# Kernel optimization log

Hardware: AMD Instinct MI355X
Metric: run time of the kernel (lower is better)

Reference implementation:

```python
import jax, jax.numpy as jnp
import numpy as np

MEL_BINS = 128
NUM_KEYS = 88
FMAX = 8000.0
HPS_HARMONICS = 3
THRESH_PCT = 85.0


def _mel_frequencies(n_mels: int, fmax: float, fmin: float = 0.0) -> np.ndarray:
    """Replicates librosa.mel_frequencies (Slaney scale, htk=False)."""
    f_sp = 200.0 / 3.0
    min_log_hz = 1000.0
    min_log_mel = min_log_hz / f_sp
    logstep = np.log(6.4) / 27.0

    def hz_to_mel(f):
        f = np.asarray(f, dtype=np.float64)
        lin = f / f_sp
        log = min_log_mel + np.log(np.maximum(f, 1e-10) / min_log_hz) / logstep
        return np.where(f >= min_log_hz, log, lin)

    def mel_to_hz(m):
        m = np.asarray(m, dtype=np.float64)
        lin = f_sp * m
        log = min_log_hz * np.exp(logstep * (m - min_log_mel))
        return np.where(m >= min_log_mel, log, lin)

    mels = np.linspace(hz_to_mel(fmin), hz_to_mel(fmax), n_mels)
    return mel_to_hz(mels)


def _compute_key_bins() -> np.ndarray:
    mel_freqs = _mel_frequencies(MEL_BINS, FMAX)  # (128,)
    pitches = np.arange(NUM_KEYS) + 21            # MIDI 21..108
    freqs = 440.0 * 2.0 ** ((pitches - 69) / 12.0)
    bins = np.argmin(np.abs(mel_freqs[None, :] - freqs[:, None]), axis=1)
    return np.minimum(bins, MEL_BINS - 1).astype(np.int32)


def setup_inputs() -> dict:
    key = jax.random.key(0)
    B, M, T = 16, MEL_BINS, 16384
    mel = jax.random.normal(key, (B, M, T), dtype=jnp.float32)
    key_bins = jnp.asarray(_compute_key_bins(), dtype=jnp.int32)  # (88,)
    return {"mel": mel, "key_bins": key_bins}


def reference(mel, key_bins):
    # mel: (B, M, T); key_bins: (88,) int32
    spec = jnp.exp(mel)                       # (B, M, T)
    hps = spec
    for h in range(2, HPS_HARMONICS + 1):
        ds = spec[:, ::h, :]                  # (B, ceil(M/h), T)
        L = ds.shape[1]
        hps = hps.at[:, :L, :].multiply(ds)   # harmonic product into low bins
    energies = jnp.take(hps, key_bins, axis=1)            # (B, 88, T)
    thresh = jnp.percentile(energies, THRESH_PCT, axis=1,
                            keepdims=True)                 # (B, 1, T)
    probs = (energies >= thresh).astype(jnp.float32)       # (B, 88, T)
    return (probs, probs)
```

## Files before the change

### kernel.cpp

```cpp
#include <hip/hip_runtime.h>

#define LOG2_T 14
#define NKEYS  88
#define NB     16
#define DMAX   64
#define TOPK   14

__global__ __launch_bounds__(256) void tsp_kernel(
    const float* __restrict__ mel,
    const int*   __restrict__ key_bins,
    float*       __restrict__ out)
{
    __shared__ int s_bin[DMAX];
    __shared__ int s_mult[DMAX];
    __shared__ int s_start[DMAX];
    __shared__ int s_Dsh;

    if (threadIdx.x == 0) {
        int D = 0, prev = -1;
        for (int k = 0; k < NKEYS; ++k) {
            int bin = key_bins[k];
            if (bin != prev && D < DMAX) {
                s_bin[D] = bin; s_mult[D] = 0; s_start[D] = k; prev = bin; ++D;
            }
            s_mult[D - 1] += 1;
        }
        for (int d = D; d < DMAX; ++d) { s_bin[d] = 0; s_mult[d] = 0; s_start[d] = NKEYS; }
        s_Dsh = D;
    }
    __syncthreads();

    const int tid = threadIdx.x;
    const int bid = blockIdx.x;
    const int b   = bid >> 6;
    const int t   = ((bid & 63) << 8) + tid;
    const int D   = s_Dsh;

    const float* melb = mel + ((size_t)b << 21);

    float e[DMAX];
    #pragma unroll
    for (int d = 0; d < DMAX; ++d) {
        const int bin = __builtin_amdgcn_readfirstlane(s_bin[d]);
        const int b1  = (2 * bin < 128) ? 2 * bin : 127;
        const int b2  = (3 * bin < 128) ? 3 * bin : 127;
        const float x0 = melb[((size_t)bin << LOG2_T) + t];
        const float x1 = melb[((size_t)b1  << LOG2_T) + t];
        const float x2 = melb[((size_t)b2  << LOG2_T) + t];
        float v = expf(x0);
        v *= (bin < 64) ? expf(x1) : 1.0f;
        v *= (bin < 43) ? expf(x2) : 1.0f;
        e[d] = (d < D) ? v : 0.0f;
    }

    float tv[TOPK];
    float cur = 1e38f;
    #pragma unroll
    for (int i = 0; i < TOPK; ++i) {
        float m = -1.0f;
        #pragma unroll
        for (int d = 0; d < DMAX; ++d) {
            const float c = (e[d] < cur) ? e[d] : -1.0f;
            m = fmaxf(m, c);
        }
        tv[i] = m;
        cur = m;
    }

    int W[TOPK];
    #pragma unroll
    for (int i = 0; i < TOPK; ++i) W[i] = 0;
    #pragma unroll
    for (int d = 0; d < DMAX; ++d) {
        const int mlt = s_mult[d];
        const float ed = e[d];
        #pragma unroll
        for (int i = 0; i < TOPK; ++i)
            W[i] += (ed >= tv[i]) ? mlt : 0;
    }
    float thr = tv[TOPK - 1];
    #pragma unroll
    for (int i = TOPK - 2; i >= 0; --i)
        thr = (W[i] >= TOPK) ? tv[i] : thr;

    float*       out2    = out + ((size_t)(NB * NKEYS) << LOG2_T);
    const size_t colbase = (((size_t)b * NKEYS) << LOG2_T) + t;
    #pragma unroll
    for (int d = 0; d < DMAX; ++d) {
        const int ks = __builtin_amdgcn_readfirstlane(s_start[d]);
        const int ke = __builtin_amdgcn_readfirstlane(s_start[d] + s_mult[d]);
        const float p = (e[d] >= thr) ? 1.0f : 0.0f;
        for (int k = ks; k < ke; ++k) {
            const size_t idx = colbase + ((size_t)k << LOG2_T);
            out[idx]  = p;
            out2[idx] = p;
        }
    }
}

extern "C" void kernel_launch(void* const* d_in, const int* in_sizes, int n_in,
                              void* d_out, int out_size, void* d_ws, size_t ws_size,
                              hipStream_t stream) {
    const float* mel = (const float*)d_in[0];
    const int*   kb  = (const int*)d_in[1];
    float*       out = (float*)d_out;
    tsp_kernel<<<dim3(1024), dim3(256), 0, stream>>>(mel, kb, out);
}
```

Measured before the change: 302.1 us.

## Batch global loads in chunks, parallelize bin setup, tree-reduce top-k max

Measured after the change: 359.5 us. 1.19x slower.

```diff
diff --git a/kernel.cpp b/kernel.cpp
--- a/kernel.cpp
+++ b/kernel.cpp
@@ -5,8 +5,9 @@
 #define NB     16
 #define DMAX   64
 #define TOPK   14
+#define CHUNK  16
 
-__global__ __launch_bounds__(256) void tsp_kernel(
+__global__ __launch_bounds__(256, 4) void tsp_kernel(
     const float* __restrict__ mel,
     const int*   __restrict__ key_bins,
     float*       __restrict__ out)
@@ -14,57 +15,96 @@
     __shared__ int s_bin[DMAX];
     __shared__ int s_mult[DMAX];
     __shared__ int s_start[DMAX];
-    __shared__ int s_Dsh;
+    __shared__ int s_wcnt[4];
 
-    if (threadIdx.x == 0) {
-        int D = 0, prev = -1;
-        for (int k = 0; k < NKEYS; ++k) {
-            int bin = key_bins[k];
-            if (bin != prev && D < DMAX) {
-                s_bin[D] = bin; s_mult[D] = 0; s_start[D] = k; prev = bin; ++D;
-            }
-            s_mult[D - 1] += 1;
+    const int tid  = threadIdx.x;
+    const int lane = tid & 63;
+    const int wid  = tid >> 6;
+
+    bool nf = false; int mybin = 0;
+    if (tid < NKEYS) {
+        mybin = key_bins[tid];
+        const int prev = tid ? key_bins[tid - 1] : -1;
+        nf = (mybin != prev);
+    }
+    const unsigned long long bm = __ballot(nf);
+    const int pre = __popcll(bm & ((1ull << lane) - 1ull));
+    if (lane == 0) s_wcnt[wid] = __popcll(bm);
+    __syncthreads();
+    if (nf) {
+        int r = pre;
+        for (int w = 0; w < wid; ++w) r += s_wcnt[w];
+        s_start[r] = tid;
+        s_bin[r]   = mybin;
+    }
+    const int D = s_wcnt[0] + s_wcnt[1];
+    __syncthreads();
+    if (tid < DMAX) {
+        if (tid < D) {
+            const int nxt = (tid == D - 1) ? NKEYS : s_start[tid + 1];
+            s_mult[tid] = nxt - s_start[tid];
+        } else {
+            s_bin[tid] = 0; s_mult[tid] = 0; s_start[tid] = NKEYS;
         }
-        for (int d = D; d < DMAX; ++d) { s_bin[d] = 0; s_mult[d] = 0; s_start[d] = NKEYS; }
-        s_Dsh = D;
     }
     __syncthreads();
 
-    const int tid = threadIdx.x;
-    const int bid = blockIdx.x;
-    const int b   = bid >> 6;
-    const int t   = ((bid & 63) << 8) + tid;
-    const int D   = s_Dsh;
-
+    const int bidx = blockIdx.x;
+    const int b    = bidx >> 6;
+    const int t    = ((bidx & 63) << 8) + tid;
     const float* melb = mel + ((size_t)b << 21);
 
     float e[DMAX];
     #pragma unroll
-    for (int d = 0; d < DMAX; ++d) {
-        const int bin = __builtin_amdgcn_readfirstlane(s_bin[d]);
-        const int b1  = (2 * bin < 128) ? 2 * bin : 127;
-        const int b2  = (3 * bin < 128) ? 3 * bin : 127;
-        const float x0 = melb[((size_t)bin << LOG2_T) + t];
-        const float x1 = melb[((size_t)b1  << LOG2_T) + t];
-        const float x2 = melb[((size_t)b2  << LOG2_T) + t];
-        float v = expf(x0);
-        v *= (bin < 64) ? expf(x1) : 1.0f;
-        v *= (bin < 43) ? expf(x2) : 1.0f;
-        e[d] = (d < D) ? v : 0.0f;
+    for (int c = 0; c < DMAX; c += CHUNK) {
+        float x0[CHUNK], x1[CHUNK], x2[CHUNK];
+        int   bns[CHUNK];
+        #pragma unroll
+        for (int i = 0; i < CHUNK; ++i) {
+            const int d  = c + i;
+            const int bn = __builtin_amdgcn_readfirstlane(s_bin[d]);
+            const int b1 = (2 * bn < 128) ? 2 * bn : 127;
+            const int b2 = (3 * bn < 128) ? 3 * bn : 127;
+            bns[i] = bn;
+            x0[i] = melb[((size_t)bn << LOG2_T) + t];
+            x1[i] = melb[((size_t)b1 << LOG2_T) + t];
+            x2[i] = melb[((size_t)b2 << LOG2_T) + t];
+        }
+        #pragma unroll
+        for (int i = 0; i < CHUNK; ++i) {
+            const int d  = c + i;
+            const int bn = bns[i];
+            float v = expf(x0[i]);
+            v *= (bn < 64) ? expf(x1[i]) : 1.0f;
+            v *= (bn < 43) ? expf(x2[i]) : 1.0f;
+            e[d] = (d < D) ? v : 0.0f;
+        }
     }
 
     float tv[TOPK];
-    float cur = 1e38f;
+    float cur = __builtin_inff();
     #pragma unroll
     for (int i = 0; i < TOPK; ++i) {
-        float m = -1.0f;
+        float t1[22];
         #pragma unroll
-        for (int d = 0; d < DMAX; ++d) {
-            const float c = (e[d] < cur) ? e[d] : -1.0f;
-            m = fmaxf(m, c);
+        for (int j = 0; j < 21; ++j) {
+            const float a0 = (e[3*j+0] < cur) ? e[3*j+0] : -1.0f;
+            const float a1 = (e[3*j+1] < cur) ? e[3*j+1] : -1.0f;
+            const float a2 = (e[3*j+2] < cur) ? e[3*j+2] : -1.0f;
+            t1[j] = fmaxf(fmaxf(a0, a1), a2);
         }
-        tv[i] = m;
-        cur = m;
+        t1[21] = (e[63] < cur) ? e[63] : -1.0f;
+        float t2[8];
+        #pragma unroll
+        for (int j = 0; j < 7; ++j)
+            t2[j] = fmaxf(fmaxf(t1[3*j], t1[3*j+1]), t1[3*j+2]);
+        t2[7] = t1[21];
+        const float t3a = fmaxf(fmaxf(t2[0], t2[1]), t2[2]);
+        const float t3b = fmaxf(fmaxf(t2[3], t2[4]), t2[5]);
+        const float t3c = fmaxf(t2[6], t2[7]);
+        const float mx  = fmaxf(fmaxf(t3a, t3b), t3c);
+        tv[i] = mx;
+        cur   = mx;
     }
 
     int W[TOPK];
@@ -72,23 +112,21 @@
     for (int i = 0; i < TOPK; ++i) W[i] = 0;
     #pragma unroll
     for (int d = 0; d < DMAX; ++d) {
-        const int mlt = s_mult[d];
-        const float ed = e[d];
+        const int   mlt = s_mult[d];
+        const float ed  = e[d];
         #pragma unroll
-        for (int i = 0; i < TOPK; ++i)
-            W[i] += (ed >= tv[i]) ? mlt : 0;
+        for (int i = 0; i < TOPK; ++i) W[i] += (ed >= tv[i]) ? mlt : 0;
     }
     float thr = tv[TOPK - 1];
     #pragma unroll
-    for (int i = TOPK - 2; i >= 0; --i)
-        thr = (W[i] >= TOPK) ? tv[i] : thr;
+    for (int i = TOPK - 2; i >= 0; --i) thr = (W[i] >= TOPK) ? tv[i] : thr;
 
     float*       out2    = out + ((size_t)(NB * NKEYS) << LOG2_T);
     const size_t colbase = (((size_t)b * NKEYS) << LOG2_T) + t;
     #pragma unroll
     for (int d = 0; d < DMAX; ++d) {
         const int ks = __builtin_amdgcn_readfirstlane(s_start[d]);
-        const int ke = __builtin_amdgcn_readfirstlane(s_start[d] + s_mult[d]);
+        const int ke = ks + __builtin_amdgcn_readfirstlane(s_mult[d]);
         const float p = (e[d] >= thr) ? 1.0f : 0.0f;
         for (int k = ks; k < ke; ++k) {
             const size_t idx = colbase + ((size_t)k << LOG2_T);
```
